# Performance work log

Measured on AMD Instinct MI355X. Metric: run time of the kernel, lower is better.

## Reference

```python
import jax, jax.numpy as jnp
import numpy as np

B, T, D = 2, 2048, 1024
DCD = 4096            # intermediate_dim
RET = 128             # expert_retrieval_dim (split into 2 halves of 64)
NEXP = 4096           # num experts (perfect square)
NKEYS = 64            # sqrt(NEXP)
H = 4                 # n_experts_heads
KPH = 8               # n_experts_per_head


def setup_inputs() -> dict:
    key = jax.random.key(0)
    ks = jax.random.split(key, 10)
    s = lambda k, shape, scale: jax.random.normal(k, shape, jnp.float32) * scale
    return {
        "hidden_states": jax.random.normal(ks[0], (B, T, D), jnp.float32),
        "Wg": s(ks[1], (D, DCD), 0.02), "bg": jnp.zeros((DCD,), jnp.float32),
        "Wu": s(ks[2], (D, DCD), 0.02), "bu": jnp.zeros((DCD,), jnp.float32),
        "Wd": s(ks[3], (DCD, D), 0.02), "bd": jnp.zeros((D,), jnp.float32),
        "Wq": s(ks[4], (D, RET * H), 0.02),          # queries proj (no bias)
        "keys": s(ks[5], (H, NKEYS, 2, RET // 2), 0.02),  # torch inits zeros; randn for a meaningful baseline
        "down_embed": s(ks[6], (NEXP, D), 0.02),
        "up_embed": s(ks[7], (NEXP, D), 0.02),
    }


def reference(hidden_states, Wg, bg, Wu, bu, Wd, bd, Wq, keys, down_embed, up_embed):
    b, t, d = hidden_states.shape
    # product-key retrieval: split query into two halves (p=2)
    q = (hidden_states @ Wq).reshape(b, t, 2, H, RET // 2)
    sim = jnp.einsum('btphn,hkpn->pbthk', q, keys)          # [2,b,t,H,NKEYS]
    sc, ix = jax.lax.top_k(sim, KPH)                        # per-half top-k
    sx, sy = sc[0], sc[1]
    ixx, ixy = ix[0], ix[1]
    all_sc = (sx[..., :, None] + sy[..., None, :]).reshape(b, t, H, KPH * KPH)
    all_ix = (ixx[..., :, None] * NKEYS + ixy[..., None, :]).reshape(b, t, H, KPH * KPH)
    scores, pk = jax.lax.top_k(all_sc, KPH)                 # [b,t,H,KPH]
    idx = jnp.take_along_axis(all_ix, pk, axis=-1)          # expert ids
    de = down_embed[idx]                                    # [b,t,H,KPH,D] gather
    ue = up_embed[idx]                                      # [b,t,H,KPH,D] gather
    w = jnp.einsum('btd,bthkd->bthk', hidden_states, de)
    w = jax.nn.silu(w) * jax.nn.softmax(scores, axis=-1)
    experts_states = jnp.einsum('bthk,bthkd->btd', w, ue)
    mlp = (jax.nn.silu(hidden_states @ Wg + bg) * (hidden_states @ Wu + bu)) @ Wd + bd
    return mlp + experts_states
```

## Files before the change

### kernel.cpp

```cpp
#include <hip/hip_runtime.h>
#include <hip/hip_bf16.h>
#include <stdint.h>

typedef unsigned short u16;
typedef __attribute__((ext_vector_type(8))) short short8;
typedef __attribute__((ext_vector_type(4))) float f32x4;

union B8 { short8 v; u16 u[8]; };
union U4 { unsigned long long q; u16 u[4]; };

__device__ __forceinline__ float b2f(u16 b) {
  union { unsigned int i; float f; } x; x.i = ((unsigned int)b) << 16; return x.f;
}
__device__ __forceinline__ u16 f2b(float f) {
  __hip_bfloat16 h = __float2bfloat16(f);
  return *reinterpret_cast<u16*>(&h);
}

#define GLOAD_LDS16(gp, lp)                                                  \
  __builtin_amdgcn_global_load_lds(                                          \
      (const __attribute__((address_space(1))) unsigned int*)(gp),           \
      (__attribute__((address_space(3))) unsigned int*)(lp), 16, 0, 0)

__global__ __launch_bounds__(256) void cvt_f2b(const float* __restrict__ src,
                                               u16* __restrict__ dst) {
  size_t i = ((size_t)blockIdx.x * 256 + threadIdx.x) * 4;
  f32x4 v = *(const f32x4*)(src + i);
  U4 o;
#pragma unroll
  for (int j = 0; j < 4; ++j) o.u[j] = f2b(v[j]);
  *(unsigned long long*)(dst + i) = o.q;
}

__global__ __launch_bounds__(256) void convt_w(const float* __restrict__ W,
                                               u16* __restrict__ WT,
                                               int K, int N) {
  int k  = blockIdx.x * 64 + (threadIdx.x & 63);
  int n8 = blockIdx.y * 32 + (threadIdx.x >> 6) * 8;
  const float* p = W + (size_t)k * N + n8;
  f32x4 a = *(const f32x4*)(p);
  f32x4 b = *(const f32x4*)(p + 4);
#pragma unroll
  for (int j = 0; j < 4; ++j) WT[(size_t)(n8 + j) * K + k] = f2b(a[j]);
#pragma unroll
  for (int j = 0; j < 4; ++j) WT[(size_t)(n8 + 4 + j) * K + k] = f2b(b[j]);
}

__global__ __launch_bounds__(256) void convt_keys(const float* __restrict__ keys,
                                                  float* __restrict__ keysT) {
  int h = blockIdx.x, p = blockIdx.y;
  int k  = threadIdx.x >> 2;
  int n0 = (threadIdx.x & 3) * 16;
  const float* src = keys + ((size_t)(h * 64 + k) * 2 + p) * 64 + n0;
  float* dst = keysT + (((size_t)h * 2 + p) * 64) * 64 + k;
#pragma unroll
  for (int c = 0; c < 16; ++c)
    dst[(size_t)(n0 + c) * 64] = src[c];
}

__global__ __launch_bounds__(256) void gemm_bf16(
    const u16* __restrict__ A, const u16* __restrict__ BT,
    const float* __restrict__ bias,
    u16* __restrict__ Cb, int M, int N, int K)
{
  __shared__ __attribute__((aligned(16))) u16 As[128 * 32];
  __shared__ __attribute__((aligned(16))) u16 Bs[128 * 32];
  int tid = threadIdx.x;
  int m0 = blockIdx.y * 128, n0 = blockIdx.x * 128;
  int wave = tid >> 6, lane = tid & 63;
  int wm = (wave >> 1) * 64, wn = (wave & 1) * 64;
  int quad = lane >> 4, r16 = lane & 15;
  int seg0 = wave * 2, seg1 = wave * 2 + 1;
  int srow = lane >> 2, scol = (lane & 3) * 8;

  const u16* a0 = A  + (size_t)(m0 + seg0 * 16 + srow) * K + scol;
  const u16* a1 = A  + (size_t)(m0 + seg1 * 16 + srow) * K + scol;
  const u16* b0 = BT + (size_t)(n0 + seg0 * 16 + srow) * K + scol;
  const u16* b1 = BT + (size_t)(n0 + seg1 * 16 + srow) * K + scol;

  f32x4 acc[4][4] = {};

  for (int k0 = 0; k0 < K; k0 += 32) {
    GLOAD_LDS16(a0 + k0, As + seg0 * 512);
    GLOAD_LDS16(a1 + k0, As + seg1 * 512);
    GLOAD_LDS16(b0 + k0, Bs + seg0 * 512);
    GLOAD_LDS16(b1 + k0, Bs + seg1 * 512);
    __syncthreads();
    short8 af[4], bfr[4];
#pragma unroll
    for (int i = 0; i < 4; ++i)
      af[i] = *(const short8*)(&As[(wm + i * 16 + r16) * 32 + quad * 8]);
#pragma unroll
    for (int j = 0; j < 4; ++j)
      bfr[j] = *(const short8*)(&Bs[(wn + j * 16 + r16) * 32 + quad * 8]);
#pragma unroll
    for (int i = 0; i < 4; ++i)
#pragma unroll
      for (int j = 0; j < 4; ++j)
        acc[i][j] = __builtin_amdgcn_mfma_f32_16x16x32_bf16(af[i], bfr[j], acc[i][j], 0, 0, 0);
    __syncthreads();
  }

#pragma unroll
  for (int i = 0; i < 4; ++i) {
    int row = m0 + wm + i * 16 + quad * 4;
#pragma unroll
    for (int j = 0; j < 4; ++j) {
      int col = n0 + wn + j * 16 + r16;
      float bv = bias ? bias[col] : 0.f;
#pragma unroll
      for (int r = 0; r < 4; ++r) {
        float v = acc[i][j][r] + bv;
        Cb[(size_t)(row + r) * N + col] = f2b(v);
      }
    }
  }
}

__global__ __launch_bounds__(256) void gemm_dsk(
    const u16* __restrict__ A, const u16* __restrict__ BT,
    float* __restrict__ P, int M, int N, int K, int Kslice, int mOff)
{
  __shared__ __attribute__((aligned(16))) u16 As[128 * 32];
  __shared__ __attribute__((aligned(16))) u16 Bs[128 * 32];
  int tid = threadIdx.x;

  int lid = blockIdx.x + blockIdx.y * gridDim.x +
            blockIdx.z * gridDim.x * gridDim.y;
  int G = gridDim.y * gridDim.z;
  int n_blk, m_blk, z_blk;
  if ((G & 7) == 0) {
    int x = lid & 7, s = lid >> 3;
    int gid = x * (G >> 3) + (s >> 3);
    n_blk = s & 7;
    m_blk = gid % gridDim.y;
    z_blk = gid / gridDim.y;
  } else {
    n_blk = blockIdx.x; m_blk = blockIdx.y; z_blk = blockIdx.z;
  }

  int m0 = m_blk * 128, n0 = n_blk * 128;
  int kb = z_blk * Kslice, ke = kb + Kslice;
  int wave = tid >> 6, lane = tid & 63;
  int wm = (wave >> 1) * 64, wn = (wave & 1) * 64;
  int quad = lane >> 4, r16 = lane & 15;
  int seg0 = wave * 2, seg1 = wave * 2 + 1;
  int srow = lane >> 2, scol = (lane & 3) * 8;

  const u16* a0 = A  + (size_t)(m0 + seg0 * 16 + srow) * K + scol;
  const u16* a1 = A  + (size_t)(m0 + seg1 * 16 + srow) * K + scol;
  const u16* b0 = BT + (size_t)(n0 + seg0 * 16 + srow) * K + scol;
  const u16* b1 = BT + (size_t)(n0 + seg1 * 16 + srow) * K + scol;

  f32x4 acc[4][4] = {};

  for (int k0 = kb; k0 < ke; k0 += 32) {
    GLOAD_LDS16(a0 + k0, As + seg0 * 512);
    GLOAD_LDS16(a1 + k0, As + seg1 * 512);
    GLOAD_LDS16(b0 + k0, Bs + seg0 * 512);
    GLOAD_LDS16(b1 + k0, Bs + seg1 * 512);
    __syncthreads();
    short8 af[4], bfr[4];
#pragma unroll
    for (int i = 0; i < 4; ++i)
      af[i] = *(const short8*)(&As[(wm + i * 16 + r16) * 32 + quad * 8]);
#pragma unroll
    for (int j = 0; j < 4; ++j)
      bfr[j] = *(const short8*)(&Bs[(wn + j * 16 + r16) * 32 + quad * 8]);
#pragma unroll
    for (int i = 0; i < 4; ++i)
#pragma unroll
      for (int j = 0; j < 4; ++j)
        acc[i][j] = __builtin_amdgcn_mfma_f32_16x16x32_bf16(af[i], bfr[j], acc[i][j], 0, 0, 0);
    __syncthreads();
  }

  float* Pz = P + (size_t)z_blk * 4194304;
#pragma unroll
  for (int i = 0; i < 4; ++i) {
    int row = mOff + m0 + wm + i * 16 + quad * 4;
#pragma unroll
    for (int j = 0; j < 4; ++j) {
      int col = n0 + wn + j * 16 + r16;
#pragma unroll
      for (int r = 0; r < 4; ++r)
        Pz[(size_t)(row + r) * N + col] = acc[i][j][r];
    }
  }
}

__global__ __launch_bounds__(256) void reduce_k(const float* __restrict__ part,
                                                int S,
                                                const float* __restrict__ es,
                                                const float* __restrict__ bd,
                                                float* __restrict__ out) {
  int t = blockIdx.x, c0 = threadIdx.x * 4;
  size_t off = (size_t)t * 1024 + c0;
  f32x4 a = *(const f32x4*)(es + off);
  for (int s = 0; s < S; ++s) {
    f32x4 p = *(const f32x4*)(part + (size_t)s * 4194304 + off);
#pragma unroll
    for (int c = 0; c < 4; ++c) a[c] += p[c];
  }
  f32x4 b = *(const f32x4*)(bd + c0);
  f32x4 o;
#pragma unroll
  for (int c = 0; c < 4; ++c) o[c] = a[c] + b[c];
  *(f32x4*)(out + off) = o;
}

__global__ __launch_bounds__(256, 2) void gemm_gu(
    const u16* __restrict__ A, const u16* __restrict__ BgT,
    const u16* __restrict__ BuT,
    const float* __restrict__ bg, const float* __restrict__ bu,
    u16* __restrict__ H, int M, int N, int K)
{
  __shared__ __attribute__((aligned(16))) u16 As[128 * 32];
  __shared__ __attribute__((aligned(16))) u16 Gs[128 * 32];
  __shared__ __attribute__((aligned(16))) u16 Us[128 * 32];
  int tid = threadIdx.x;
  int m0 = blockIdx.y * 128, n0 = blockIdx.x * 128;
  int wave = tid >> 6, lane = tid & 63;
  int wm = (wave >> 1) * 64, wn = (wave & 1) * 64;
  int quad = lane >> 4, r16 = lane & 15;
  int seg0 = wave * 2, seg1 = wave * 2 + 1;
  int srow = lane >> 2, scol = (lane & 3) * 8;

  const u16* a0 = A   + (size_t)(m0 + seg0 * 16 + srow) * K + scol;
  const u16* a1 = A   + (size_t)(m0 + seg1 * 16 + srow) * K + scol;
  const u16* g0 = BgT + (size_t)(n0 + seg0 * 16 + srow) * K + scol;
  const u16* g1 = BgT + (size_t)(n0 + seg1 * 16 + srow) * K + scol;
  const u16* u0 = BuT + (size_t)(n0 + seg0 * 16 + srow) * K + scol;
  const u16* u1 = BuT + (size_t)(n0 + seg1 * 16 + srow) * K + scol;

  f32x4 ag[4][4] = {}, au[4][4] = {};

  for (int k0 = 0; k0 < K; k0 += 32) {
    GLOAD_LDS16(a0 + k0, As + seg0 * 512);
    GLOAD_LDS16(a1 + k0, As + seg1 * 512);
    GLOAD_LDS16(g0 + k0, Gs + seg0 * 512);
    GLOAD_LDS16(g1 + k0, Gs + seg1 * 512);
    GLOAD_LDS16(u0 + k0, Us + seg0 * 512);
    GLOAD_LDS16(u1 + k0, Us + seg1 * 512);
    __syncthreads();
    short8 af[4], bfr[4];
#pragma unroll
    for (int i = 0; i < 4; ++i)
      af[i] = *(const short8*)(&As[(wm + i * 16 + r16) * 32 + quad * 8]);
#pragma unroll
    for (int j = 0; j < 4; ++j)
      bfr[j] = *(const short8*)(&Gs[(wn + j * 16 + r16) * 32 + quad * 8]);
#pragma unroll
    for (int i = 0; i < 4; ++i)
#pragma unroll
      for (int j = 0; j < 4; ++j)
        ag[i][j] = __builtin_amdgcn_mfma_f32_16x16x32_bf16(af[i], bfr[j], ag[i][j], 0, 0, 0);
#pragma unroll
    for (int j = 0; j < 4; ++j)
      bfr[j] = *(const short8*)(&Us[(wn + j * 16 + r16) * 32 + quad * 8]);
#pragma unroll
    for (int i = 0; i < 4; ++i)
#pragma unroll
      for (int j = 0; j < 4; ++j)
        au[i][j] = __builtin_amdgcn_mfma_f32_16x16x32_bf16(af[i], bfr[j], au[i][j], 0, 0, 0);
    __syncthreads();
  }

#pragma unroll
  for (int i = 0; i < 4; ++i) {
    int row = m0 + wm + i * 16 + quad * 4;
#pragma unroll
    for (int j = 0; j < 4; ++j) {
      int col = n0 + wn + j * 16 + r16;
      float bgv = bg[col], buv = bu[col];
#pragma unroll
      for (int r = 0; r < 4; ++r) {
        float g = ag[i][j][r] + bgv;
        float u = au[i][j][r] + buv;
        float h = (g / (1.f + __expf(-g))) * u;
        H[(size_t)(row + r) * N + col] = f2b(h);
      }
    }
  }
}

template<int NP>
__device__ __forceinline__ void sort8_desc(float (&v)[NP], int (&ii)[NP], int j) {
#pragma unroll
  for (int k = 2; k <= 8; k <<= 1) {
#pragma unroll
    for (int s = k >> 1; s > 0; s >>= 1) {
      bool desc  = (j & k) == 0;
      bool lower = (j & s) == 0;
#pragma unroll
      for (int p = 0; p < NP; ++p) {
        float vp = __shfl_xor(v[p], s);
        int   ip = __shfl_xor(ii[p], s);
        bool mf = (v[p] > vp) || (v[p] == vp && ii[p] < ip);
        bool keep = (desc == lower) ? mf : !mf;
        if (!keep) { v[p] = vp; ii[p] = ip; }
      }
    }
  }
}

template<int NP>
__device__ __forceinline__ void merge_top8(float (&v)[NP], int (&ii)[NP], int j) {
#pragma unroll
  for (int r = 0; r < 3; ++r) {
    int mask = (8 << r) | 7;
#pragma unroll
    for (int p = 0; p < NP; ++p) {
      float vp = __shfl_xor(v[p], mask);
      int   ip = __shfl_xor(ii[p], mask);
      bool mf = (v[p] > vp) || (v[p] == vp && ii[p] < ip);
      if (!mf) { v[p] = vp; ii[p] = ip; }
    }
#pragma unroll
    for (int s = 4; s > 0; s >>= 1) {
      bool lower = (j & s) == 0;
#pragma unroll
      for (int p = 0; p < NP; ++p) {
        float vq = __shfl_xor(v[p], s);
        int   iq = __shfl_xor(ii[p], s);
        bool mf = (v[p] > vq) || (v[p] == vq && ii[p] < iq);
        bool keep = lower ? mf : !mf;
        if (!keep) { v[p] = vq; ii[p] = iq; }
      }
    }
  }
}

__global__ __launch_bounds__(256) void retrieve_k(
    const u16*  __restrict__ q,
    const float* __restrict__ keysT,
    int* __restrict__ idx_out,
    float* __restrict__ p_out)
{
  int t = blockIdx.x;
  int w = threadIdx.x >> 6, lane = threadIdx.x & 63;
  int j = lane & 7;

  float v[2]; int ii[2];
#pragma unroll
  for (int p = 0; p < 2; ++p) {
    const u16*   qp = q + (size_t)t * 512 + p * 256 + w * 64;
    const float* kp = keysT + ((size_t)(w * 2 + p) * 64) * 64 + lane;
    float s0 = 0.f, s1 = 0.f, s2 = 0.f, s3 = 0.f;
#pragma unroll
    for (int n = 0; n < 64; n += 8) {
      B8 qv; qv.v = *(const short8*)(qp + n);
      s0 += b2f(qv.u[0]) * kp[(size_t)(n + 0) * 64];
      s1 += b2f(qv.u[1]) * kp[(size_t)(n + 1) * 64];
      s2 += b2f(qv.u[2]) * kp[(size_t)(n + 2) * 64];
      s3 += b2f(qv.u[3]) * kp[(size_t)(n + 3) * 64];
      s0 += b2f(qv.u[4]) * kp[(size_t)(n + 4) * 64];
      s1 += b2f(qv.u[5]) * kp[(size_t)(n + 5) * 64];
      s2 += b2f(qv.u[6]) * kp[(size_t)(n + 6) * 64];
      s3 += b2f(qv.u[7]) * kp[(size_t)(n + 7) * 64];
    }
    v[p] = (s0 + s1) + (s2 + s3); ii[p] = lane;
  }

  sort8_desc<2>(v, ii, j);
  merge_top8<2>(v, ii, j);

  float v2[1] = { __shfl(v[0], lane >> 3) + __shfl(v[1], lane & 7) };
  int  pos[1] = { lane };
  merge_top8<1>(v2, pos, j);

  int ex = __shfl(ii[0], pos[0] >> 3);
  int ey = __shfl(ii[1], pos[0] & 7);

  float m = __shfl(v2[0], 0);
  float e = __expf(v2[0] - m);
  float sum = e;
#pragma unroll
  for (int s = 4; s > 0; s >>= 1) sum += __shfl_xor(sum, s);

  if (lane < 8) {
    int o = (t * 4 + w) * 8 + lane;
    p_out[o]   = e / sum;
    idx_out[o] = ex * 64 + ey;
  }
}

__global__ __launch_bounds__(256) void expert_k(
    const u16* __restrict__ xb, const u16* __restrict__ downb,
    const u16* __restrict__ upb,
    const int* __restrict__ idx, const float* __restrict__ probs,
    float* __restrict__ es)
{
  __shared__ float acc_s[4][1024];
  int t = blockIdx.x;
  int w = threadIdx.x >> 6, lane = threadIdx.x & 63;
  const size_t tb = (size_t)t * 1024;
  const int lo = lane * 8;

  B8 xv0, xv1;
  xv0.v = *(const short8*)(xb + tb + lo);
  xv1.v = *(const short8*)(xb + tb + 512 + lo);
  float xf[16];
#pragma unroll
  for (int c = 0; c < 8; ++c) { xf[c] = b2f(xv0.u[c]); xf[8 + c] = b2f(xv1.u[c]); }

  float a[16] = {};
#pragma unroll
  for (int e8 = 0; e8 < 8; ++e8) {
    int e = w * 8 + e8;
    int id = idx[t * 32 + e];
    const u16* dp = downb + (size_t)id * 1024;
    B8 d0, d1;
    d0.v = *(const short8*)(dp + lo);
    d1.v = *(const short8*)(dp + 512 + lo);
    float part = 0.f;
#pragma unroll
    for (int c = 0; c < 8; ++c)
      part += xf[c] * b2f(d0.u[c]) + xf[8 + c] * b2f(d1.u[c]);
#pragma unroll
    for (int off = 32; off; off >>= 1) part += __shfl_xor(part, off);
    float gate = (part / (1.f + __expf(-part))) * probs[t * 32 + e];
    const u16* upp = upb + (size_t)id * 1024;
    B8 u0, u1;
    u0.v = *(const short8*)(upp + lo);
    u1.v = *(const short8*)(upp + 512 + lo);
#pragma unroll
    for (int c = 0; c < 8; ++c) {
      a[c]     += gate * b2f(u0.u[c]);
      a[8 + c] += gate * b2f(u1.u[c]);
    }
  }
#pragma unroll
  for (int c = 0; c < 8; ++c) {
    acc_s[w][lo + c]       = a[c];
    acc_s[w][512 + lo + c] = a[8 + c];
  }
  __syncthreads();
  int d0i = threadIdx.x * 4;
  f32x4 s0 = *(const f32x4*)(&acc_s[0][d0i]);
  f32x4 s1 = *(const f32x4*)(&acc_s[1][d0i]);
  f32x4 s2 = *(const f32x4*)(&acc_s[2][d0i]);
  f32x4 s3 = *(const f32x4*)(&acc_s[3][d0i]);
  f32x4 o;
#pragma unroll
  for (int c = 0; c < 4; ++c) o[c] = (s0[c] + s1[c]) + (s2[c] + s3[c]);
  *(f32x4*)(es + tb + d0i) = o;
}

extern "C" void kernel_launch(void* const* d_in, const int* in_sizes, int n_in,
                              void* d_out, int out_size, void* d_ws, size_t ws_size,
                              hipStream_t stream)
{
  const float* x    = (const float*)d_in[0];
  const float* Wg   = (const float*)d_in[1];
  const float* bg   = (const float*)d_in[2];
  const float* Wu   = (const float*)d_in[3];
  const float* bu   = (const float*)d_in[4];
  const float* Wd   = (const float*)d_in[5];
  const float* bd   = (const float*)d_in[6];
  const float* Wq   = (const float*)d_in[7];
  const float* keys = (const float*)d_in[8];
  const float* down = (const float*)d_in[9];
  const float* up   = (const float*)d_in[10];
  float* out = (float*)d_out;

  const size_t MB = 1048576;
  char* ws = (char*)d_ws;
  u16*   xb    = (u16*)(ws);
  u16*   WgT   = (u16*)(ws + 8  * MB);
  u16*   WuT   = (u16*)(ws + 16 * MB);
  u16*   WdT   = (u16*)(ws + 24 * MB);
  float* es    = (float*)(ws + 32 * MB);
  u16*   WqT   = (u16*)(ws + 32 * MB);
  u16*   qb    = (u16*)(ws + 34 * MB);
  float* keysT = (float*)(ws + 47 * MB);
  int*   idxb  = (int*)(ws + 48 * MB);
  float* prb   = (float*)(ws + 48 * MB + 512 * 1024);
  u16*   downb = (u16*)(ws + 49 * MB);
  u16*   upb   = (u16*)(ws + 57 * MB);

  int S = 2;
  while (S > 1 && 65 * MB + (size_t)S * 16 * MB + 1 * MB > ws_size) S >>= 1;
  float* part = (float*)(ws + 65 * MB);
  size_t gboff = 65 * MB + (size_t)S * 16 * MB;
  u16*   gb    = (u16*)(ws + gboff);

  size_t avail = ws_size > gboff ? ws_size - gboff : 0;
  int rows = 4096;
  while (rows > 128 && (size_t)rows * 4096 * 2 > avail) rows >>= 1;
  int Ksl = 4096 / S;

  cvt_f2b<<<4096, 256, 0, stream>>>(x, xb);
  cvt_f2b<<<4096, 256, 0, stream>>>(down, downb);
  cvt_f2b<<<4096, 256, 0, stream>>>(up, upb);
  convt_w<<<dim3(16, 16),  256, 0, stream>>>(Wq, WqT, 1024, 512);
  convt_w<<<dim3(16, 128), 256, 0, stream>>>(Wg, WgT, 1024, 4096);
  convt_w<<<dim3(16, 128), 256, 0, stream>>>(Wu, WuT, 1024, 4096);
  convt_w<<<dim3(64, 32),  256, 0, stream>>>(Wd, WdT, 4096, 1024);
  convt_keys<<<dim3(4, 2), 256, 0, stream>>>(keys, keysT);

  gemm_bf16<<<dim3(4, 32), 256, 0, stream>>>(xb, WqT, nullptr,
                                             qb, 4096, 512, 1024);
  retrieve_k<<<4096, 256, 0, stream>>>(qb, keysT, idxb, prb);
  expert_k<<<4096, 256, 0, stream>>>(xb, downb, upb, idxb, prb, es);

  for (int m0c = 0; m0c < 4096; m0c += rows) {
    int gy = rows / 128;
    gemm_gu<<<dim3(32, gy), 256, 0, stream>>>(xb + (size_t)m0c * 1024, WgT, WuT,
                                              bg, bu, gb, rows, 4096, 1024);
    gemm_dsk<<<dim3(8, gy, S), 256, 0, stream>>>(gb, WdT, part,
                                                 rows, 1024, 4096, Ksl, m0c);
  }
  reduce_k<<<4096, 256, 0, stream>>>(part, S, es, bd, out);
}
```

Measured before the change: 432.1 us.

## Split fused gate/up GEMM into two single-output GEMMs with grouped block ordering

Replaces the fused gate+up GEMM, which held two accumulator sets per block, with two passes of a single-output GEMM. The first pass writes the up projection to a bf16 buffer, and the second computes the gate and applies SiLU times the stored up value in its epilogue. The new kernel also remaps block IDs into grouped chunks to improve L2 reuse. It drops the workspace-size-dependent chunking and split choice and assumes a fixed large workspace, at the cost of an extra 32MB intermediate write and read and one more launch.

```diff
diff --git a/kernel.cpp b/kernel.cpp
--- a/kernel.cpp
+++ b/kernel.cpp
@@ -117,6 +117,87 @@
   }
 }
 
+__global__ __launch_bounds__(256) void gemm_eb(
+    const u16* __restrict__ A, const u16* __restrict__ BT,
+    const float* __restrict__ bias, const u16* __restrict__ U,
+    u16* __restrict__ C, int M, int N, int K, int mode)
+{
+  __shared__ __attribute__((aligned(16))) u16 As[128 * 32];
+  __shared__ __attribute__((aligned(16))) u16 Bs[128 * 32];
+  int tid = threadIdx.x;
+
+  int lid = blockIdx.y * gridDim.x + blockIdx.x;
+  int total = gridDim.x * gridDim.y;
+  int n_blk, m_blk;
+  if ((total & 63) == 0 && (gridDim.x & 7) == 0) {
+    int x = lid & 7, s = lid >> 3;
+    int gid = x * (total >> 6) + (s >> 3);
+    int nch = gid / gridDim.y;
+    m_blk = gid % gridDim.y;
+    n_blk = nch * 8 + (s & 7);
+  } else {
+    n_blk = blockIdx.x; m_blk = blockIdx.y;
+  }
+
+  int m0 = m_blk * 128, n0 = n_blk * 128;
+  int wave = tid >> 6, lane = tid & 63;
+  int wm = (wave >> 1) * 64, wn = (wave & 1) * 64;
+  int quad = lane >> 4, r16 = lane & 15;
+  int seg0 = wave * 2, seg1 = wave * 2 + 1;
+  int srow = lane >> 2, scol = (lane & 3) * 8;
+
+  const u16* a0 = A  + (size_t)(m0 + seg0 * 16 + srow) * K + scol;
+  const u16* a1 = A  + (size_t)(m0 + seg1 * 16 + srow) * K + scol;
+  const u16* b0 = BT + (size_t)(n0 + seg0 * 16 + srow) * K + scol;
+  const u16* b1 = BT + (size_t)(n0 + seg1 * 16 + srow) * K + scol;
+
+  f32x4 acc[4][4] = {};
+
+  for (int k0 = 0; k0 < K; k0 += 32) {
+    GLOAD_LDS16(a0 + k0, As + seg0 * 512);
+    GLOAD_LDS16(a1 + k0, As + seg1 * 512);
+    GLOAD_LDS16(b0 + k0, Bs + seg0 * 512);
+    GLOAD_LDS16(b1 + k0, Bs + seg1 * 512);
+    __syncthreads();
+    short8 af[4], bfr[4];
+#pragma unroll
+    for (int i = 0; i < 4; ++i)
+      af[i] = *(const short8*)(&As[(wm + i * 16 + r16) * 32 + quad * 8]);
+#pragma unroll
+    for (int j = 0; j < 4; ++j)
+      bfr[j] = *(const short8*)(&Bs[(wn + j * 16 + r16) * 32 + quad * 8]);
+#pragma unroll
+    for (int i = 0; i < 4; ++i)
+#pragma unroll
+      for (int j = 0; j < 4; ++j)
+        acc[i][j] = __builtin_amdgcn_mfma_f32_16x16x32_bf16(af[i], bfr[j], acc[i][j], 0, 0, 0);
+    __syncthreads();
+  }
+
+#pragma unroll
+  for (int i = 0; i < 4; ++i) {
+    int row0 = m0 + wm + i * 16 + quad * 4;
+#pragma unroll
+    for (int j = 0; j < 4; ++j) {
+      int col = n0 + wn + j * 16 + r16;
+      float bv = bias[col];
+#pragma unroll
+      for (int r = 0; r < 4; ++r) {
+        int row = row0 + r;
+        float g = acc[i][j][r] + bv;
+        float h;
+        if (mode == 1) {
+          float u = b2f(U[(size_t)row * N + col]);
+          h = (g / (1.f + __expf(-g))) * u;
+        } else {
+          h = g;
+        }
+        C[(size_t)row * N + col] = f2b(h);
+      }
+    }
+  }
+}
+
 __global__ __launch_bounds__(256) void gemm_dsk(
     const u16* __restrict__ A, const u16* __restrict__ BT,
     float* __restrict__ P, int M, int N, int K, int Kslice, int mOff)
@@ -207,81 +288,6 @@
 #pragma unroll
   for (int c = 0; c < 4; ++c) o[c] = a[c] + b[c];
   *(f32x4*)(out + off) = o;
-}
-
-__global__ __launch_bounds__(256, 2) void gemm_gu(
-    const u16* __restrict__ A, const u16* __restrict__ BgT,
-    const u16* __restrict__ BuT,
-    const float* __restrict__ bg, const float* __restrict__ bu,
-    u16* __restrict__ H, int M, int N, int K)
-{
-  __shared__ __attribute__((aligned(16))) u16 As[128 * 32];
-  __shared__ __attribute__((aligned(16))) u16 Gs[128 * 32];
-  __shared__ __attribute__((aligned(16))) u16 Us[128 * 32];
-  int tid = threadIdx.x;
-  int m0 = blockIdx.y * 128, n0 = blockIdx.x * 128;
-  int wave = tid >> 6, lane = tid & 63;
-  int wm = (wave >> 1) * 64, wn = (wave & 1) * 64;
-  int quad = lane >> 4, r16 = lane & 15;
-  int seg0 = wave * 2, seg1 = wave * 2 + 1;
-  int srow = lane >> 2, scol = (lane & 3) * 8;
-
-  const u16* a0 = A   + (size_t)(m0 + seg0 * 16 + srow) * K + scol;
-  const u16* a1 = A   + (size_t)(m0 + seg1 * 16 + srow) * K + scol;
-  const u16* g0 = BgT + (size_t)(n0 + seg0 * 16 + srow) * K + scol;
-  const u16* g1 = BgT + (size_t)(n0 + seg1 * 16 + srow) * K + scol;
-  const u16* u0 = BuT + (size_t)(n0 + seg0 * 16 + srow) * K + scol;
-  const u16* u1 = BuT + (size_t)(n0 + seg1 * 16 + srow) * K + scol;
-
-  f32x4 ag[4][4] = {}, au[4][4] = {};
-
-  for (int k0 = 0; k0 < K; k0 += 32) {
-    GLOAD_LDS16(a0 + k0, As + seg0 * 512);
-    GLOAD_LDS16(a1 + k0, As + seg1 * 512);
-    GLOAD_LDS16(g0 + k0, Gs + seg0 * 512);
-    GLOAD_LDS16(g1 + k0, Gs + seg1 * 512);
-    GLOAD_LDS16(u0 + k0, Us + seg0 * 512);
-    GLOAD_LDS16(u1 + k0, Us + seg1 * 512);
-    __syncthreads();
-    short8 af[4], bfr[4];
-#pragma unroll
-    for (int i = 0; i < 4; ++i)
-      af[i] = *(const short8*)(&As[(wm + i * 16 + r16) * 32 + quad * 8]);
-#pragma unroll
-    for (int j = 0; j < 4; ++j)
-      bfr[j] = *(const short8*)(&Gs[(wn + j * 16 + r16) * 32 + quad * 8]);
-#pragma unroll
-    for (int i = 0; i < 4; ++i)
-#pragma unroll
-      for (int j = 0; j < 4; ++j)
-        ag[i][j] = __builtin_amdgcn_mfma_f32_16x16x32_bf16(af[i], bfr[j], ag[i][j], 0, 0, 0);
-#pragma unroll
-    for (int j = 0; j < 4; ++j)
-      bfr[j] = *(const short8*)(&Us[(wn + j * 16 + r16) * 32 + quad * 8]);
-#pragma unroll
-    for (int i = 0; i < 4; ++i)
-#pragma unroll
-      for (int j = 0; j < 4; ++j)
-        au[i][j] = __builtin_amdgcn_mfma_f32_16x16x32_bf16(af[i], bfr[j], au[i][j], 0, 0, 0);
-    __syncthreads();
-  }
-
-#pragma unroll
-  for (int i = 0; i < 4; ++i) {
-    int row = m0 + wm + i * 16 + quad * 4;
-#pragma unroll
-    for (int j = 0; j < 4; ++j) {
-      int col = n0 + wn + j * 16 + r16;
-      float bgv = bg[col], buv = bu[col];
-#pragma unroll
-      for (int r = 0; r < 4; ++r) {
-        float g = ag[i][j][r] + bgv;
-        float u = au[i][j][r] + buv;
-        float h = (g / (1.f + __expf(-g))) * u;
-        H[(size_t)(row + r) * N + col] = f2b(h);
-      }
-    }
-  }
 }
 
 template<int NP>
@@ -478,17 +484,10 @@
   float* prb   = (float*)(ws + 48 * MB + 512 * 1024);
   u16*   downb = (u16*)(ws + 49 * MB);
   u16*   upb   = (u16*)(ws + 57 * MB);
-
-  int S = 2;
-  while (S > 1 && 65 * MB + (size_t)S * 16 * MB + 1 * MB > ws_size) S >>= 1;
-  float* part = (float*)(ws + 65 * MB);
-  size_t gboff = 65 * MB + (size_t)S * 16 * MB;
-  u16*   gb    = (u16*)(ws + gboff);
-
-  size_t avail = ws_size > gboff ? ws_size - gboff : 0;
-  int rows = 4096;
-  while (rows > 128 && (size_t)rows * 4096 * 2 > avail) rows >>= 1;
-  int Ksl = 4096 / S;
+  float* part  = (float*)(ws + 65 * MB);
+  u16*   Ub    = (u16*)(ws + 97 * MB);
+  u16*   gb    = (u16*)(ws + 129 * MB);
+  const int S = 2;
 
   cvt_f2b<<<4096, 256, 0, stream>>>(x, xb);
   cvt_f2b<<<4096, 256, 0, stream>>>(down, downb);
@@ -504,12 +503,11 @@
   retrieve_k<<<4096, 256, 0, stream>>>(qb, keysT, idxb, prb);
   expert_k<<<4096, 256, 0, stream>>>(xb, downb, upb, idxb, prb, es);
 
-  for (int m0c = 0; m0c < 4096; m0c += rows) {
-    int gy = rows / 128;
-    gemm_gu<<<dim3(32, gy), 256, 0, stream>>>(xb + (size_t)m0c * 1024, WgT, WuT,
-                                              bg, bu, gb, rows, 4096, 1024);
-    gemm_dsk<<<dim3(8, gy, S), 256, 0, stream>>>(gb, WdT, part,
-                                                 rows, 1024, 4096, Ksl, m0c);
-  }
+  gemm_eb<<<dim3(32, 32), 256, 0, stream>>>(xb, WuT, bu, nullptr, Ub,
+                                            4096, 4096, 1024, 0);
+  gemm_eb<<<dim3(32, 32), 256, 0, stream>>>(xb, WgT, bg, Ub, gb,
+                                            4096, 4096, 1024, 1);
+  gemm_dsk<<<dim3(8, 32, S), 256, 0, stream>>>(gb, WdT, part,
+                                               4096, 1024, 4096, 4096 / S, 0);
   reduce_k<<<4096, 256, 0, stream>>>(part, S, es, bd, out);
 }
```

Result: slower. 492.1 us (+13.9%).
